# Optimization experiments

Measured on AMD Instinct MI355X. Metric: run time of the kernel, lower is better.

## Reference

```python
import jax, jax.numpy as jnp
import numpy as np

B, S, D = 4, 2048, 768
H = 12
HD = D // H  # 64
EPS = 1e-12  # F.normalize eps


def setup_inputs() -> dict:
    key = jax.random.key(0)
    ks = jax.random.split(key, 6)
    scale = 1.0 / np.sqrt(D)
    x = jax.random.normal(ks[0], (B, S, D), dtype=jnp.float32)
    Wq = jax.random.normal(ks[1], (D, D), dtype=jnp.float32) * scale
    Wk = jax.random.normal(ks[2], (D, D), dtype=jnp.float32) * scale
    Wv = jax.random.normal(ks[3], (D, D), dtype=jnp.float32) * scale
    Wo = jax.random.normal(ks[4], (D, D), dtype=jnp.float32) * scale
    temperature = jnp.ones((H, 1, 1), dtype=jnp.float32)
    return {"x": x, "Wq": Wq, "Wk": Wk, "Wv": Wv, "Wo": Wo, "temperature": temperature}


def _heads(t):
    # [B,S,D] -> [B,H,S,HD]
    return t.reshape(B, S, H, HD).transpose(0, 2, 1, 3)


def reference(x, Wq, Wk, Wv, Wo, temperature):
    # Linear weights stored torch-style [out,in]: y = x @ W.T
    q = _heads(x @ Wq.T)
    k = _heads(x @ Wk.T)
    v = _heads(x @ Wv.T)
    # cosine-sim normalize (F.normalize: x / max(||x||, eps))
    q = q / jnp.maximum(jnp.linalg.norm(q, axis=-1, keepdims=True), EPS)
    k = k / jnp.maximum(jnp.linalg.norm(k, axis=-1, keepdims=True), EPS)
    # [B,H,S,S] scores with per-head learnable temperature
    attn = jnp.einsum("bhqd,bhkd->bhqk", q, k) * temperature  # temperature broadcasts [H,1,1]
    causal = jnp.tril(jnp.ones((S, S), dtype=bool))
    attn = jnp.where(causal, attn, -jnp.inf)
    attn = jax.nn.softmax(attn, axis=-1)
    out = jnp.einsum("bhqk,bhkd->bhqd", attn, v)
    out = out.transpose(0, 2, 1, 3).reshape(B, S, D)
    return out @ Wo.T
```

## Files before the change

### kernel.cpp

```cpp
#include <hip/hip_runtime.h>
#include <hip/hip_bf16.h>

#define B_ 4
#define S_ 2048
#define D_ 768
#define H_ 12
#define HD_ 64
#define M_ (B_*S_)
#define LOG2E 1.44269504088896f

typedef __attribute__((ext_vector_type(8))) short bf8;
typedef __attribute__((ext_vector_type(4))) float f4;
typedef unsigned short u16;
typedef unsigned int   u32;

typedef __attribute__((address_space(3))) u32 lds_u32;
typedef __attribute__((address_space(1))) const u32 glob_u32;

__device__ __forceinline__ float bf2f(u16 u) {
  union { u32 i; float f; } c; c.i = ((u32)u) << 16; return c.f;
}
__device__ __forceinline__ u16 f2bf(float x) {
  union { float f; u32 i; } c; c.f = x;
  u32 r = (c.i + 0x7FFFu + ((c.i >> 16) & 1u)) >> 16;
  return (u16)r;
}
__device__ __forceinline__ u16 cvt_bf16(float x) {
  u32 r;
  asm("v_cvt_pk_bf16_f32 %0, %1, %1" : "=v"(r) : "v"(x));
  return (u16)r;
}
__device__ __forceinline__ float exp2_raw(float x) {
  float r;
  asm("v_exp_f32 %0, %1" : "=v"(r) : "v"(x));
  return r;
}
__device__ __forceinline__ void glds16(const u16* g, u16* l) {
  __builtin_amdgcn_global_load_lds((glob_u32*)g, (lds_u32*)l, 16, 0, 0);
}

__global__ __launch_bounds__(256) void stage_all(const float* __restrict__ x,
                                                 const float* __restrict__ w0, const float* __restrict__ w1,
                                                 const float* __restrict__ w2, const float* __restrict__ w3,
                                                 u16* __restrict__ xo,
                                                 u16* __restrict__ o0, u16* __restrict__ o1,
                                                 u16* __restrict__ o2, u16* __restrict__ o3,
                                                 int nx4, int nw4)
{
  int y = blockIdx.y;
  const float* src = (y == 0) ? x : (y == 1) ? w0 : (y == 2) ? w1 : (y == 3) ? w2 : w3;
  u16*         dst = (y == 0) ? xo : (y == 1) ? o0 : (y == 2) ? o1 : (y == 3) ? o2 : o3;
  int n4 = (y == 0) ? nx4 : nw4;
  for (int i = blockIdx.x * blockDim.x + threadIdx.x; i < n4; i += gridDim.x * blockDim.x) {
    float4 v = ((const float4*)src)[i];
    ushort4 o;
    o.x = f2bf(v.x); o.y = f2bf(v.y); o.z = f2bf(v.z); o.w = f2bf(v.w);
    ((ushort4*)dst)[i] = o;
  }
}

__global__ __launch_bounds__(256) void stage_cvt(const float* __restrict__ in,
                                                 u16* __restrict__ out, int n4)
{
  for (int i = blockIdx.x * blockDim.x + threadIdx.x; i < n4; i += gridDim.x * blockDim.x) {
    float4 v = ((const float4*)in)[i];
    ushort4 o;
    o.x = f2bf(v.x); o.y = f2bf(v.y); o.z = f2bf(v.z); o.w = f2bf(v.w);
    ((ushort4*)out)[i] = o;
  }
}

__device__ __forceinline__ bf8 ldcvt8(const float* __restrict__ p) {
  float4 a = *(const float4*)p;
  float4 b = *(const float4*)(p + 4);
  bf8 r;
  r[0] = f2bf(a.x); r[1] = f2bf(a.y); r[2] = f2bf(a.z); r[3] = f2bf(a.w);
  r[4] = f2bf(b.x); r[5] = f2bf(b.y); r[6] = f2bf(b.z); r[7] = f2bf(b.w);
  return r;
}

#define MFMA_BF16 __builtin_amdgcn_mfma_f32_16x16x32_bf16

template <int EPI>
__device__ __forceinline__ void gemm_core(u16* a_lds, u16* b_lds,
                                          int row0, int col0,
                                          const u16* __restrict__ A,
                                          const u16* __restrict__ W,
                                          u16* __restrict__ Cb,
                                          float* __restrict__ Cf,
                                          const float* __restrict__ temp)
{
  const int w  = threadIdx.x >> 6;
  const int ln = threadIdx.x & 63;
  const int li = ln & 15, g = ln >> 4;
  const int wr = w >> 1, wc = w & 1;

  const int srow = ln >> 3;
  const int scol = ((ln & 7) ^ srow) * 8;
  const u16* Abase = A + (size_t)(row0 + srow) * 768 + scol;
  const u16* Bbase = W + (size_t)(col0 + srow) * 768 + scol;

  f4 acc[2][4];
#pragma unroll
  for (int i = 0; i < 2; ++i)
#pragma unroll
    for (int j = 0; j < 4; ++j) acc[i][j] = (f4){0.f, 0.f, 0.f, 0.f};

  for (int kt = 0; kt < 12; ++kt) {
    const int k0 = kt * 64;
#pragma unroll
    for (int i = 0; i < 2; ++i) {
      int seg = w * 2 + i;
      glds16(Abase + (size_t)(seg * 8) * 768 + k0, a_lds + seg * 512);
    }
#pragma unroll
    for (int i = 0; i < 4; ++i) {
      int seg = w * 4 + i;
      glds16(Bbase + (size_t)(seg * 8) * 768 + k0, b_lds + seg * 512);
    }
    asm volatile("s_waitcnt vmcnt(0)" ::: "memory");
    __syncthreads();

#pragma unroll
    for (int kk = 0; kk < 2; ++kk) {
      const int co = (((kk * 4 + g) ^ (li & 7)) * 8);
      bf8 a0 = *(const bf8*)(a_lds + (wr * 32 + li) * 64 + co);
      bf8 a1 = *(const bf8*)(a_lds + (wr * 32 + 16 + li) * 64 + co);
      bf8 b0 = *(const bf8*)(b_lds + (wc * 64 + li) * 64 + co);
      bf8 b1 = *(const bf8*)(b_lds + (wc * 64 + 16 + li) * 64 + co);
      bf8 b2 = *(const bf8*)(b_lds + (wc * 64 + 32 + li) * 64 + co);
      bf8 b3 = *(const bf8*)(b_lds + (wc * 64 + 48 + li) * 64 + co);
      acc[0][0] = MFMA_BF16(a0, b0, acc[0][0], 0, 0, 0);
      acc[0][1] = MFMA_BF16(a0, b1, acc[0][1], 0, 0, 0);
      acc[0][2] = MFMA_BF16(a0, b2, acc[0][2], 0, 0, 0);
      acc[0][3] = MFMA_BF16(a0, b3, acc[0][3], 0, 0, 0);
      acc[1][0] = MFMA_BF16(a1, b0, acc[1][0], 0, 0, 0);
      acc[1][1] = MFMA_BF16(a1, b1, acc[1][1], 0, 0, 0);
      acc[1][2] = MFMA_BF16(a1, b2, acc[1][2], 0, 0, 0);
      acc[1][3] = MFMA_BF16(a1, b3, acc[1][3], 0, 0, 0);
    }
    __syncthreads();
  }

  const int wrow0 = row0 + wr * 32;
  const int wcol0 = col0 + wc * 64;

  if (EPI == 1 || EPI == 2) {
    float tmul = 1.0f;
    if (EPI == 2) tmul = temp[wcol0 >> 6] * LOG2E;
#pragma unroll
    for (int i = 0; i < 2; ++i)
#pragma unroll
      for (int r = 0; r < 4; ++r) {
        float ss = 0.f;
#pragma unroll
        for (int j = 0; j < 4; ++j) ss += acc[i][j][r] * acc[i][j][r];
#pragma unroll
        for (int msk = 1; msk < 16; msk <<= 1) ss += __shfl_xor(ss, msk, 64);
        float scl = tmul / fmaxf(sqrtf(ss), 1e-12f);
#pragma unroll
        for (int j = 0; j < 4; ++j) acc[i][j][r] *= scl;
      }
  }

#pragma unroll
  for (int i = 0; i < 2; ++i)
#pragma unroll
    for (int j = 0; j < 4; ++j)
#pragma unroll
      for (int r = 0; r < 4; ++r) {
        int row = wrow0 + i * 16 + g * 4 + r;
        int col = wcol0 + j * 16 + li;
        if (EPI == 3) Cf[(size_t)row * 768 + col] = acc[i][j][r];
        else          Cb[(size_t)row * 768 + col] = f2bf(acc[i][j][r]);
      }
}

__global__ __launch_bounds__(256) void gemm_qkv(const u16* __restrict__ XB,
                                                const u16* __restrict__ Wq, const u16* __restrict__ Wk,
                                                const u16* __restrict__ Wv,
                                                u16* __restrict__ Qb, u16* __restrict__ Kb,
                                                u16* __restrict__ Vb,
                                                const float* __restrict__ temp)
{
  __shared__ __align__(16) u16 a_lds[64 * 64];
  __shared__ __align__(16) u16 b_lds[128 * 64];
  const int bid  = blockIdx.x;
  const int xcd  = bid & 7;
  const int j    = bid >> 3;
  const int row0 = (xcd * 16 + j / 18) * 64;
  const int rest = j % 18;
  const int z    = rest / 6;
  const int col0 = (rest % 6) * 128;
  if (z == 0)      gemm_core<2>(a_lds, b_lds, row0, col0, XB, Wq, Qb, nullptr, temp);
  else if (z == 1) gemm_core<1>(a_lds, b_lds, row0, col0, XB, Wk, Kb, nullptr, temp);
  else             gemm_core<0>(a_lds, b_lds, row0, col0, XB, Wv, Vb, nullptr, temp);
}

__global__ __launch_bounds__(256) void gemm_out(const u16* __restrict__ A,
                                                const u16* __restrict__ W,
                                                float* __restrict__ Cf)
{
  __shared__ __align__(16) u16 a_lds[64 * 64];
  __shared__ __align__(16) u16 b_lds[128 * 64];
  const int bid  = blockIdx.x;
  const int xcd  = bid & 7;
  const int j    = bid >> 3;
  const int row0 = (xcd * 16 + j / 6) * 64;
  const int col0 = (j % 6) * 128;
  gemm_core<3>(a_lds, b_lds, row0, col0, A, W, nullptr, Cf, nullptr);
}

template <int EPI>
__global__ __launch_bounds__(256) void gemm_wf32(const u16* __restrict__ A,
                                                 const float* __restrict__ W,
                                                 u16* __restrict__ Cb,
                                                 float* __restrict__ Cf,
                                                 const float* __restrict__ temp)
{
  const int w  = threadIdx.x >> 6;
  const int ln = threadIdx.x & 63;
  const int li = ln & 15, g = ln >> 4;
  const int wr = w >> 1, wc = w & 1;
  const int row0 = blockIdx.x * 64 + wr * 32;
  const int col0 = blockIdx.y * 128 + wc * 64;

  const u16*   Ap = A + (size_t)(row0 + li) * 768 + g * 8;
  const float* Wp = W + (size_t)(col0 + li) * 768 + g * 8;

  f4 acc[2][4];
#pragma unroll
  for (int i = 0; i < 2; ++i)
#pragma unroll
    for (int j = 0; j < 4; ++j) acc[i][j] = (f4){0.f, 0.f, 0.f, 0.f};

  for (int k = 0; k < 768; k += 32) {
    bf8 a0 = *(const bf8*)(Ap + k);
    bf8 a1 = *(const bf8*)(Ap + (size_t)16 * 768 + k);
    bf8 b0 = ldcvt8(Wp + k);
    bf8 b1 = ldcvt8(Wp + (size_t)16 * 768 + k);
    bf8 b2 = ldcvt8(Wp + (size_t)32 * 768 + k);
    bf8 b3 = ldcvt8(Wp + (size_t)48 * 768 + k);
    acc[0][0] = MFMA_BF16(a0, b0, acc[0][0], 0, 0, 0);
    acc[0][1] = MFMA_BF16(a0, b1, acc[0][1], 0, 0, 0);
    acc[0][2] = MFMA_BF16(a0, b2, acc[0][2], 0, 0, 0);
    acc[0][3] = MFMA_BF16(a0, b3, acc[0][3], 0, 0, 0);
    acc[1][0] = MFMA_BF16(a1, b0, acc[1][0], 0, 0, 0);
    acc[1][1] = MFMA_BF16(a1, b1, acc[1][1], 0, 0, 0);
    acc[1][2] = MFMA_BF16(a1, b2, acc[1][2], 0, 0, 0);
    acc[1][3] = MFMA_BF16(a1, b3, acc[1][3], 0, 0, 0);
  }

  if (EPI == 1 || EPI == 2) {
    float tmul = 1.0f;
    if (EPI == 2) tmul = temp[col0 >> 6] * LOG2E;
#pragma unroll
    for (int i = 0; i < 2; ++i)
#pragma unroll
      for (int r = 0; r < 4; ++r) {
        float ss = 0.f;
#pragma unroll
        for (int j = 0; j < 4; ++j) ss += acc[i][j][r] * acc[i][j][r];
#pragma unroll
        for (int msk = 1; msk < 16; msk <<= 1) ss += __shfl_xor(ss, msk, 64);
        float scl = tmul / fmaxf(sqrtf(ss), 1e-12f);
#pragma unroll
        for (int j = 0; j < 4; ++j) acc[i][j][r] *= scl;
      }
  }

#pragma unroll
  for (int i = 0; i < 2; ++i)
#pragma unroll
    for (int j = 0; j < 4; ++j)
#pragma unroll
      for (int r = 0; r < 4; ++r) {
        int row = row0 + i * 16 + g * 4 + r;
        int col = col0 + j * 16 + li;
        if (EPI == 3) Cf[(size_t)row * 768 + col] = acc[i][j][r];
        else          Cb[(size_t)row * 768 + col] = f2bf(acc[i][j][r]);
      }
}

__global__ __launch_bounds__(256, 4) void flash_attn(const u16* __restrict__ Q,
                                                     const u16* __restrict__ K,
                                                     const u16* __restrict__ V,
                                                     u16* __restrict__ O,
                                                     const float* __restrict__ temp)
{
  const int bid = blockIdx.x;
  const int xcd = bid & 7;
  const int j   = bid >> 3;
  const int bh  = xcd * 6 + j % 6;
  const int qt  = 31 - j / 6;
  const int b = bh / H_, h = bh % H_;
  const size_t base = (size_t)b * S_ * D_ + h * HD_;
  const u16* Qp = Q + base;
  const u16* Kp = K + base;
  const u16* Vp = V + base;
  u16*       Op = O + base;

  const float C2 = fabsf(temp[h]) * LOG2E;

  const int w  = threadIdx.x >> 6;
  const int ln = threadIdx.x & 63;
  const int li = ln & 15, g = ln >> 4;

  __shared__ __align__(16) u16 k_lds[64][72];
  __shared__ __align__(16) u16 vt[64][72];
  __shared__ __align__(16) u16 p_lds[4][16][72];

  const int q0 = qt * 64;
  const int qrow = q0 + w * 16 + li;

  bf8 qf0 = *(const bf8*)(Qp + (size_t)qrow * D_ + g * 8);
  bf8 qf1 = *(const bf8*)(Qp + (size_t)qrow * D_ + 32 + g * 8);

  const int key2 = (threadIdx.x >> 3) * 2;
  const int d0   = (threadIdx.x & 7) * 8;
  const u16* ksrc = Kp + (size_t)key2 * D_ + d0;
  const u16* vsrc = Vp + (size_t)key2 * D_ + d0;

  bf8 ka = *(const bf8*)(ksrc);
  bf8 kb = *(const bf8*)(ksrc + D_);
  bf8 va = *(const bf8*)(vsrc);
  bf8 vb_ = *(const bf8*)(vsrc + D_);

  f4 o[4];
  float lp[4] = {0.f, 0.f, 0.f, 0.f};
#pragma unroll
  for (int c = 0; c < 4; ++c) o[c] = (f4){0.f, 0.f, 0.f, 0.f};

  for (int kt = 0; kt <= qt; ++kt) {
    __syncthreads();
    {
      *(bf8*)&k_lds[key2][d0]     = ka;
      *(bf8*)&k_lds[key2 + 1][d0] = kb;
#pragma unroll
      for (int j2 = 0; j2 < 8; ++j2) {
        ushort2 pr;
        pr.x = (u16)va[j2]; pr.y = (u16)vb_[j2];
        *(ushort2*)&vt[d0 + j2][key2 ^ d0] = pr;
      }
    }
    if (kt < qt) {
      const u16* ks = ksrc + (size_t)(kt + 1) * 64 * D_;
      const u16* vs = vsrc + (size_t)(kt + 1) * 64 * D_;
      ka  = *(const bf8*)(ks);
      kb  = *(const bf8*)(ks + D_);
      va  = *(const bf8*)(vs);
      vb_ = *(const bf8*)(vs + D_);
    }
    asm volatile("s_waitcnt lgkmcnt(0)" ::: "memory");
    __builtin_amdgcn_s_barrier();

    f4 sc[4];
#pragma unroll
    for (int c = 0; c < 4; ++c) sc[c] = (f4){0.f, 0.f, 0.f, 0.f};
#pragma unroll
    for (int c = 0; c < 4; ++c) {
      bf8 k0 = *(const bf8*)&k_lds[c * 16 + li][g * 8];
      bf8 k1 = *(const bf8*)&k_lds[c * 16 + li][32 + g * 8];
      sc[c] = MFMA_BF16(qf0, k0, sc[c], 0, 0, 0);
      sc[c] = MFMA_BF16(qf1, k1, sc[c], 0, 0, 0);
    }

    if (kt == qt) {
#pragma unroll
      for (int c = 0; c < 4; ++c)
#pragma unroll
        for (int r = 0; r < 4; ++r) {
          int col = kt * 64 + c * 16 + li;
          int row = q0 + w * 16 + g * 4 + r;
          if (col > row) sc[c][r] = -__builtin_inff();
        }
    }

#pragma unroll
    for (int c = 0; c < 4; ++c)
#pragma unroll
      for (int r = 0; r < 4; ++r) {
        float p = exp2_raw(sc[c][r] - C2);
        sc[c][r] = p;
        lp[r] += p;
      }

#pragma unroll
    for (int c = 0; c < 4; ++c)
#pragma unroll
      for (int r = 0; r < 4; ++r)
        p_lds[w][g * 4 + r][(c * 16 + li) ^ (g << 3)] = cvt_bf16(sc[c][r]);

#pragma unroll
    for (int ks = 0; ks < 2; ++ks) {
      bf8 pa = *(const bf8*)&p_lds[w][li][(ks * 32 + g * 8) ^ ((li >> 2) << 3)];
#pragma unroll
      for (int c = 0; c < 4; ++c) {
        int d  = c * 16 + li;
        int kbx = (ks * 32 + g * 8) ^ (d & 56);
        bf8 vv = *(const bf8*)&vt[d][kbx];
        o[c] = MFMA_BF16(pa, vv, o[c], 0, 0, 0);
      }
    }
  }

  float l[4];
#pragma unroll
  for (int r = 0; r < 4; ++r) {
    float s = lp[r];
#pragma unroll
    for (int msk = 1; msk < 16; msk <<= 1) s += __shfl_xor(s, msk, 64);
    l[r] = 1.0f / s;
  }
#pragma unroll
  for (int c = 0; c < 4; ++c)
#pragma unroll
    for (int r = 0; r < 4; ++r) {
      int row = q0 + w * 16 + g * 4 + r;
      Op[(size_t)row * D_ + c * 16 + li] = cvt_bf16(o[c][r] * l[r]);
    }
}

extern "C" void kernel_launch(void* const* d_in, const int* in_sizes, int n_in,
                              void* d_out, int out_size, void* d_ws, size_t ws_size,
                              hipStream_t stream) {
  const void *xv, *Wqv, *Wkv, *Wvv, *Wov, *tv;
  if (in_sizes[0] == M_ * D_) {
    xv = d_in[0]; Wqv = d_in[1]; Wkv = d_in[2]; Wvv = d_in[3]; Wov = d_in[4]; tv = d_in[5];
  } else {
    Wkv = d_in[0]; Wov = d_in[1]; Wqv = d_in[2]; Wvv = d_in[3]; tv = d_in[4]; xv = d_in[5];
  }
  const float* x    = (const float*)xv;
  const float* Wq   = (const float*)Wqv;
  const float* Wk   = (const float*)Wkv;
  const float* Wv   = (const float*)Wvv;
  const float* Wo   = (const float*)Wov;
  const float* temp = (const float*)tv;

  const size_t SZ  = (size_t)M_ * D_;
  const size_t WSZ = (size_t)D_ * D_;
  u16* ws = (u16*)d_ws;
  u16* Qb = ws;
  u16* Kb = ws + SZ;
  u16* Vb = ws + 2 * SZ;
  u16* XB = (u16*)d_out;

  const bool stageW = ws_size >= (3 * SZ + 4 * WSZ) * sizeof(u16);
  u16* Wqb = ws + 3 * SZ;
  u16* Wkb = Wqb + WSZ;
  u16* Wvb = Wkb + WSZ;
  u16* Wob = Wvb + WSZ;

  if (stageW) {
    stage_all<<<dim3(512, 5), 256, 0, stream>>>(x, Wq, Wk, Wv, Wo,
                                                XB, Wqb, Wkb, Wvb, Wob,
                                                (int)(SZ / 4), (int)(WSZ / 4));
    gemm_qkv<<<2304, 256, 0, stream>>>(XB, Wqb, Wkb, Wvb, Qb, Kb, Vb, temp);
    flash_attn<<<1536, 256, 0, stream>>>(Qb, Kb, Vb, Qb, temp);
    gemm_out<<<768, 256, 0, stream>>>(Qb, Wob, (float*)d_out);
  } else {
    dim3 gg(M_ / 64, D_ / 128), bb(256);
    stage_cvt<<<2048, 256, 0, stream>>>(x, XB, (int)(SZ / 4));
    gemm_wf32<2><<<gg, bb, 0, stream>>>(XB, Wq, Qb, nullptr, temp);
    gemm_wf32<1><<<gg, bb, 0, stream>>>(XB, Wk, Kb, nullptr, temp);
    gemm_wf32<0><<<gg, bb, 0, stream>>>(XB, Wv, Vb, nullptr, temp);
    flash_attn<<<1536, 256, 0, stream>>>(Qb, Kb, Vb, Qb, temp);
    gemm_wf32<3><<<gg, bb, 0, stream>>>(Qb, Wo, nullptr, (float*)d_out, temp);
  }
}
```

Before: 127.1 us.

## Write V transposed from QKV GEMM to drop in-kernel V transpose in attention

The V projection epilogue now stages its tile through LDS and writes V in a per-head transposed [B*H, 64, S] layout. The attention kernel can then load V tiles as contiguous rows straight into LDS, with no per-element transpose scatter and no XOR swizzle. This removes scalar ushort2 LDS stores from every key-tile iteration of the attention loop. In exchange the GEMM epilogue gains extra LDS traffic and two barriers, the merged LDS buffer grows, and the unswizzled vt reads may hit bank conflicts.

```diff
diff --git a/kernel.cpp b/kernel.cpp
--- a/kernel.cpp
+++ b/kernel.cpp
@@ -82,14 +82,16 @@
 #define MFMA_BF16 __builtin_amdgcn_mfma_f32_16x16x32_bf16
 
 template <int EPI>
-__device__ __forceinline__ void gemm_core(u16* a_lds, u16* b_lds,
-                                          int row0, int col0,
+__device__ __forceinline__ void gemm_core(u16* lds, int row0, int col0,
                                           const u16* __restrict__ A,
                                           const u16* __restrict__ W,
                                           u16* __restrict__ Cb,
                                           float* __restrict__ Cf,
                                           const float* __restrict__ temp)
 {
+  u16* a_lds = lds;
+  u16* b_lds = lds + 64 * 64;
+
   const int w  = threadIdx.x >> 6;
   const int ln = threadIdx.x & 63;
   const int li = ln & 15, g = ln >> 4;
@@ -163,6 +165,34 @@
       }
   }
 
+  if (EPI == 4) {
+    __syncthreads();
+#pragma unroll
+    for (int i = 0; i < 2; ++i)
+#pragma unroll
+      for (int j = 0; j < 4; ++j)
+#pragma unroll
+        for (int r = 0; r < 4; ++r) {
+          int cl = wc * 64 + j * 16 + li;
+          int rl = wr * 32 + i * 16 + g * 4 + r;
+          lds[cl * 64 + rl] = cvt_bf16(acc[i][j][r]);
+        }
+    __syncthreads();
+    const int sb = row0 & 2047;
+    const int bb = row0 >> 11;
+#pragma unroll
+    for (int q = 0; q < 4; ++q) {
+      int c2 = threadIdx.x * 4 + q;
+      int cl = c2 >> 3;
+      int s8 = (c2 & 7) * 8;
+      int colg = col0 + cl;
+      int bh = bb * H_ + (colg >> 6);
+      int d  = colg & 63;
+      *(bf8*)(Cb + ((size_t)bh * 64 + d) * 2048 + sb + s8) = *(const bf8*)&lds[cl * 64 + s8];
+    }
+    return;
+  }
+
 #pragma unroll
   for (int i = 0; i < 2; ++i)
 #pragma unroll
@@ -180,11 +210,10 @@
                                                 const u16* __restrict__ Wq, const u16* __restrict__ Wk,
                                                 const u16* __restrict__ Wv,
                                                 u16* __restrict__ Qb, u16* __restrict__ Kb,
-                                                u16* __restrict__ Vb,
+                                                u16* __restrict__ Vt,
                                                 const float* __restrict__ temp)
 {
-  __shared__ __align__(16) u16 a_lds[64 * 64];
-  __shared__ __align__(16) u16 b_lds[128 * 64];
+  __shared__ __align__(16) u16 lds[192 * 64];
   const int bid  = blockIdx.x;
   const int xcd  = bid & 7;
   const int j    = bid >> 3;
@@ -192,23 +221,22 @@
   const int rest = j % 18;
   const int z    = rest / 6;
   const int col0 = (rest % 6) * 128;
-  if (z == 0)      gemm_core<2>(a_lds, b_lds, row0, col0, XB, Wq, Qb, nullptr, temp);
-  else if (z == 1) gemm_core<1>(a_lds, b_lds, row0, col0, XB, Wk, Kb, nullptr, temp);
-  else             gemm_core<0>(a_lds, b_lds, row0, col0, XB, Wv, Vb, nullptr, temp);
+  if (z == 0)      gemm_core<2>(lds, row0, col0, XB, Wq, Qb, nullptr, temp);
+  else if (z == 1) gemm_core<1>(lds, row0, col0, XB, Wk, Kb, nullptr, temp);
+  else             gemm_core<4>(lds, row0, col0, XB, Wv, Vt, nullptr, temp);
 }
 
 __global__ __launch_bounds__(256) void gemm_out(const u16* __restrict__ A,
                                                 const u16* __restrict__ W,
                                                 float* __restrict__ Cf)
 {
-  __shared__ __align__(16) u16 a_lds[64 * 64];
-  __shared__ __align__(16) u16 b_lds[128 * 64];
+  __shared__ __align__(16) u16 lds[192 * 64];
   const int bid  = blockIdx.x;
   const int xcd  = bid & 7;
   const int j    = bid >> 3;
   const int row0 = (xcd * 16 + j / 6) * 64;
   const int col0 = (j % 6) * 128;
-  gemm_core<3>(a_lds, b_lds, row0, col0, A, W, nullptr, Cf, nullptr);
+  gemm_core<3>(lds, row0, col0, A, W, nullptr, Cf, nullptr);
 }
 
 template <int EPI>
@@ -277,14 +305,16 @@
       for (int r = 0; r < 4; ++r) {
         int row = row0 + i * 16 + g * 4 + r;
         int col = col0 + j * 16 + li;
-        if (EPI == 3) Cf[(size_t)row * 768 + col] = acc[i][j][r];
-        else          Cb[(size_t)row * 768 + col] = f2bf(acc[i][j][r]);
+        if (EPI == 3)      Cf[(size_t)row * 768 + col] = acc[i][j][r];
+        else if (EPI == 0) Cb[((size_t)((row >> 11) * H_ + (col >> 6)) * 64 + (col & 63)) * 2048
+                              + (row & 2047)] = f2bf(acc[i][j][r]);
+        else               Cb[(size_t)row * 768 + col] = f2bf(acc[i][j][r]);
       }
 }
 
 __global__ __launch_bounds__(256, 4) void flash_attn(const u16* __restrict__ Q,
                                                      const u16* __restrict__ K,
-                                                     const u16* __restrict__ V,
+                                                     const u16* __restrict__ Vt,
                                                      u16* __restrict__ O,
                                                      const float* __restrict__ temp)
 {
@@ -295,10 +325,10 @@
   const int qt  = 31 - j / 6;
   const int b = bh / H_, h = bh % H_;
   const size_t base = (size_t)b * S_ * D_ + h * HD_;
-  const u16* Qp = Q + base;
-  const u16* Kp = K + base;
-  const u16* Vp = V + base;
-  u16*       Op = O + base;
+  const u16* Qp  = Q + base;
+  const u16* Kp  = K + base;
+  const u16* Vtp = Vt + (size_t)bh * 64 * 2048;
+  u16*       Op  = O + base;
 
   const float C2 = fabsf(temp[h]) * LOG2E;
 
@@ -316,15 +346,15 @@
   bf8 qf0 = *(const bf8*)(Qp + (size_t)qrow * D_ + g * 8);
   bf8 qf1 = *(const bf8*)(Qp + (size_t)qrow * D_ + 32 + g * 8);
 
-  const int key2 = (threadIdx.x >> 3) * 2;
-  const int d0   = (threadIdx.x & 7) * 8;
-  const u16* ksrc = Kp + (size_t)key2 * D_ + d0;
-  const u16* vsrc = Vp + (size_t)key2 * D_ + d0;
+  const int r2 = (threadIdx.x >> 3) * 2;
+  const int c0 = (threadIdx.x & 7) * 8;
+  const u16* ksrc = Kp  + (size_t)r2 * D_ + c0;
+  const u16* vsrc = Vtp + (size_t)r2 * 2048 + c0;
 
   bf8 ka = *(const bf8*)(ksrc);
   bf8 kb = *(const bf8*)(ksrc + D_);
   bf8 va = *(const bf8*)(vsrc);
-  bf8 vb_ = *(const bf8*)(vsrc + D_);
+  bf8 vb_ = *(const bf8*)(vsrc + 2048);
 
   f4 o[4];
   float lp[4] = {0.f, 0.f, 0.f, 0.f};
@@ -334,22 +364,18 @@
   for (int kt = 0; kt <= qt; ++kt) {
     __syncthreads();
     {
-      *(bf8*)&k_lds[key2][d0]     = ka;
-      *(bf8*)&k_lds[key2 + 1][d0] = kb;
-#pragma unroll
-      for (int j2 = 0; j2 < 8; ++j2) {
-        ushort2 pr;
-        pr.x = (u16)va[j2]; pr.y = (u16)vb_[j2];
-        *(ushort2*)&vt[d0 + j2][key2 ^ d0] = pr;
-      }
+      *(bf8*)&k_lds[r2][c0]     = ka;
+      *(bf8*)&k_lds[r2 + 1][c0] = kb;
+      *(bf8*)&vt[r2][c0]        = va;
+      *(bf8*)&vt[r2 + 1][c0]    = vb_;
     }
     if (kt < qt) {
       const u16* ks = ksrc + (size_t)(kt + 1) * 64 * D_;
-      const u16* vs = vsrc + (size_t)(kt + 1) * 64 * D_;
+      const u16* vs = vsrc + (kt + 1) * 64;
       ka  = *(const bf8*)(ks);
       kb  = *(const bf8*)(ks + D_);
       va  = *(const bf8*)(vs);
-      vb_ = *(const bf8*)(vs + D_);
+      vb_ = *(const bf8*)(vs + 2048);
     }
     asm volatile("s_waitcnt lgkmcnt(0)" ::: "memory");
     __builtin_amdgcn_s_barrier();
@@ -396,9 +422,7 @@
       bf8 pa = *(const bf8*)&p_lds[w][li][(ks * 32 + g * 8) ^ ((li >> 2) << 3)];
 #pragma unroll
       for (int c = 0; c < 4; ++c) {
-        int d  = c * 16 + li;
-        int kbx = (ks * 32 + g * 8) ^ (d & 56);
-        bf8 vv = *(const bf8*)&vt[d][kbx];
+        bf8 vv = *(const bf8*)&vt[c * 16 + li][ks * 32 + g * 8];
         o[c] = MFMA_BF16(pa, vv, o[c], 0, 0, 0);
       }
     }
@@ -442,7 +466,7 @@
   u16* ws = (u16*)d_ws;
   u16* Qb = ws;
   u16* Kb = ws + SZ;
-  u16* Vb = ws + 2 * SZ;
+  u16* Vt = ws + 2 * SZ;
   u16* XB = (u16*)d_out;
 
   const bool stageW = ws_size >= (3 * SZ + 4 * WSZ) * sizeof(u16);
@@ -455,16 +479,16 @@
     stage_all<<<dim3(512, 5), 256, 0, stream>>>(x, Wq, Wk, Wv, Wo,
                                                 XB, Wqb, Wkb, Wvb, Wob,
                                                 (int)(SZ / 4), (int)(WSZ / 4));
-    gemm_qkv<<<2304, 256, 0, stream>>>(XB, Wqb, Wkb, Wvb, Qb, Kb, Vb, temp);
-    flash_attn<<<1536, 256, 0, stream>>>(Qb, Kb, Vb, Qb, temp);
+    gemm_qkv<<<2304, 256, 0, stream>>>(XB, Wqb, Wkb, Wvb, Qb, Kb, Vt, temp);
+    flash_attn<<<1536, 256, 0, stream>>>(Qb, Kb, Vt, Qb, temp);
     gemm_out<<<768, 256, 0, stream>>>(Qb, Wob, (float*)d_out);
   } else {
     dim3 gg(M_ / 64, D_ / 128), bb(256);
     stage_cvt<<<2048, 256, 0, stream>>>(x, XB, (int)(SZ / 4));
     gemm_wf32<2><<<gg, bb, 0, stream>>>(XB, Wq, Qb, nullptr, temp);
     gemm_wf32<1><<<gg, bb, 0, stream>>>(XB, Wk, Kb, nullptr, temp);
-    gemm_wf32<0><<<gg, bb, 0, stream>>>(XB, Wv, Vb, nullptr, temp);
-    flash_attn<<<1536, 256, 0, stream>>>(Qb, Kb, Vb, Qb, temp);
+    gemm_wf32<0><<<gg, bb, 0, stream>>>(XB, Wv, Vt, nullptr, temp);
+    flash_attn<<<1536, 256, 0, stream>>>(Qb, Kb, Vt, Qb, temp);
     gemm_wf32<3><<<gg, bb, 0, stream>>>(Qb, Wo, nullptr, (float*)d_out, temp);
   }
 }
```

After: 130.5 us. +2.7%, slower.
